# Kernel tuning notes

Hardware: AMD Instinct MI355X
Metric: run time of the kernel (lower is better)

Reference implementation:

```python
import jax, jax.numpy as jnp
import numpy as np

D_MODEL = 1024
D_FF = 4 * D_MODEL
N = D_MODEL * D_FF          # 4,194,304 == 2**22, so pad_n == N (no padding)
PAD_N = N
FFT_LEN = PAD_N // 2 + 1    # 2,097,153 rfft bins
KEEP = int(FFT_LEN * 0.25)  # 524,288 kept coefficients ('medium')
B, S = 4, 2048


def _decompress(cr, ci, idx, shape, scale):
    # scatter top-k complex coeffs into full rfft spectrum, inverse rfft,
    # reshape to weight matrix and rescale (riemann_decompress)
    coeffs = jax.lax.complex(cr, ci)                      # complex64 [KEEP]
    full = jnp.zeros((FFT_LEN,), jnp.complex64).at[idx].set(coeffs)
    w = jnp.fft.irfft(full, n=PAD_N)                      # [PAD_N] real
    return w.reshape(shape) * scale                       # scale is [1], broadcasts


def setup_inputs() -> dict:
    key = jax.random.key(0)
    ks = jax.random.split(key, 9)
    return {
        "x": jax.random.normal(ks[0], (B, S, D_MODEL), jnp.float32),
        "c_fc_coeffs_real": jax.random.normal(ks[1], (KEEP,), jnp.float32),
        "c_fc_coeffs_imag": jax.random.normal(ks[2], (KEEP,), jnp.float32),
        "c_fc_indices": jnp.arange(KEEP, dtype=jnp.int32),
        "c_fc_scale": jax.random.uniform(ks[3], (1,), jnp.float32, 0.5, 1.5),
        "c_fc_bias": jax.random.normal(ks[4], (D_FF,), jnp.float32),
        "c_proj_coeffs_real": jax.random.normal(ks[5], (KEEP,), jnp.float32),
        "c_proj_coeffs_imag": jax.random.normal(ks[6], (KEEP,), jnp.float32),
        "c_proj_indices": jnp.arange(KEEP, dtype=jnp.int32),
        "c_proj_scale": jax.random.uniform(ks[7], (1,), jnp.float32, 0.5, 1.5),
        "c_proj_bias": jax.random.normal(ks[8], (D_MODEL,), jnp.float32),
    }


def reference(x, c_fc_coeffs_real, c_fc_coeffs_imag, c_fc_indices, c_fc_scale,
              c_fc_bias, c_proj_coeffs_real, c_proj_coeffs_imag, c_proj_indices,
              c_proj_scale, c_proj_bias):
    # c_fc.weight stored [d_model, d_ff]; F.linear(x, W.T) == x @ W
    w_fc = _decompress(c_fc_coeffs_real, c_fc_coeffs_imag, c_fc_indices,
                       (D_MODEL, D_FF), c_fc_scale)
    h = jnp.einsum('bsd,df->bsf', x, w_fc) + c_fc_bias
    h = jax.nn.gelu(h, approximate=False)  # nn.GELU() exact erf form
    w_proj = _decompress(c_proj_coeffs_real, c_proj_coeffs_imag, c_proj_indices,
                         (D_FF, D_MODEL), c_proj_scale)
    return jnp.einsum('bsf,fd->bsd', h, w_proj) + c_proj_bias
```

## Files before the change

### kernel.cpp

```cpp
#include <hip/hip_runtime.h>
#include <hip/hip_bf16.h>
#include <hip/hip_fp8.h>
#include <math.h>

#define M_HALF 2097152
#define W_SCALE 256.0f

typedef __bf16 bf16_t;
typedef unsigned char u8;
typedef __attribute__((ext_vector_type(4))) float f32x4;
typedef __attribute__((ext_vector_type(2))) long long2v;

#define GLOBAL_AS __attribute__((address_space(1)))
#define LDS_AS    __attribute__((address_space(3)))

__device__ __forceinline__ u8 to_fp8(float v) {
    __hip_fp8_e4m3 t(v);
    return *reinterpret_cast<u8*>(&t);
}

__device__ __forceinline__ int perm8(int g) {
    return (((g >> 3) * 4 + (g & 3)) << 1) + ((g >> 2) & 1);
}
__device__ __forceinline__ int permk(int k) {
    return (k & ~127) | (perm8((k >> 3) & 15) * 8 + (k & 7));
}

__device__ __forceinline__ float2 cadd(float2 a, float2 b){ return make_float2(a.x+b.x, a.y+b.y); }
__device__ __forceinline__ float2 csub(float2 a, float2 b){ return make_float2(a.x-b.x, a.y-b.y); }
__device__ __forceinline__ float2 cmul(float2 a, float2 b){ return make_float2(a.x*b.x-a.y*b.y, a.x*b.y+a.y*b.x); }
__device__ __forceinline__ float2 cmuli(float2 a){ return make_float2(-a.y, a.x); }

__device__ __forceinline__ void radix8_inv(const float2 v[8], float2 X[8]) {
    const float cc = 0.70710678118654752f;
    float2 a0 = cadd(v[0], v[4]), a1 = cadd(v[1], v[5]), a2 = cadd(v[2], v[6]), a3 = cadd(v[3], v[7]);
    float2 b0 = csub(v[0], v[4]), b1 = csub(v[1], v[5]), b2 = csub(v[2], v[6]), b3 = csub(v[3], v[7]);
    b1 = cmul(b1, make_float2(cc, cc));
    b2 = cmuli(b2);
    b3 = cmul(b3, make_float2(-cc, cc));
    float2 c0 = cadd(a0, a2), c1 = cadd(a1, a3), d0 = csub(a0, a2), d1 = cmuli(csub(a1, a3));
    float2 e0 = cadd(b0, b2), e1 = cadd(b1, b3), f0 = csub(b0, b2), f1 = cmuli(csub(b1, b3));
    X[0] = cadd(c0, c1); X[4] = csub(c0, c1); X[2] = cadd(d0, d1); X[6] = csub(d0, d1);
    X[1] = cadd(e0, e1); X[5] = csub(e0, e1); X[3] = cadd(f0, f1); X[7] = csub(f0, f1);
}


__global__ __launch_bounds__(256) void zero2_kernel(float2* p, int n) {
    int i = blockIdx.x*256 + threadIdx.x;
    if (i < n) p[i] = make_float2(0.f, 0.f);
}

__global__ __launch_bounds__(256) void scatter2_kernel(const float* __restrict__ crA,
                                                       const float* __restrict__ ciA,
                                                       const int* __restrict__ idxA,
                                                       const float* __restrict__ crB,
                                                       const float* __restrict__ ciB,
                                                       const int* __restrict__ idxB,
                                                       float2* __restrict__ specA,
                                                       float2* __restrict__ specB, int keep) {
    int i = blockIdx.x*256 + threadIdx.x;
    if (i < keep) {
        int k = idxA[i];
        long pos = (k < M_HALF) ? ((long)(k & 511)*4096 + (k >> 9)) : (long)M_HALF;
        specA[pos] = make_float2(crA[i], ciA[i]);
    } else if (i < 2*keep) {
        int t = i - keep;
        int k = idxB[t];
        long pos = (k < M_HALF) ? ((long)(k & 511)*4096 + (k >> 9)) : (long)M_HALF;
        specB[pos] = make_float2(crB[t], ciB[t]);
    }
}


__global__ __launch_bounds__(512) void ifft_p4096_dual(const float2* __restrict__ specTA,
                                                       const float2* __restrict__ specTB,
                                                       float2* __restrict__ dstA,
                                                       float2* __restrict__ dstB,
                                                       const float* __restrict__ scaleA,
                                                       const float* __restrict__ scaleB) {
    __shared__ float2 L[8*656];
    int bb = blockIdx.x;
    const float2* spec; float2* dst; const float* scale;
    if (bb < 512) { spec = specTA; dst = dstA; scale = scaleA; }
    else          { bb -= 512; spec = specTB; dst = dstB; scale = scaleB; }
    const int j = bb;
    const int x = threadIdx.x;
    const float s = scale[0] * (1.0f/(float)M_HALF);
    float2 v[8];
    {
        float ang0 = (float)(3.14159265358979323846 * (double)(j + 512*x) / 2097152.0);
        float sn, cs; sincosf(ang0, &sn, &cs);
        const float2 step = make_float2(0.98078528040323044913f,
                                        0.19509032201612826785f);
        float2 tw = make_float2(cs, sn);
        const long arow = (long)j * 4096;
        const long brow = (long)(512 - j) * 4096;
#pragma unroll
        for (int u = 0; u < 8; ++u) {
            int t = x + 512*u;
            float2 a = spec[arow + t];
            float2 b;
            if (j == 0) b = (t == 0) ? spec[(long)M_HALF] : spec[4096 - t];
            else        b = spec[brow + 4095 - t];
            if (j == 0 && t == 0) { a.y = 0.0f; b.y = 0.0f; }
            float Er = 0.5f*(a.x + b.x), Ei = 0.5f*(a.y - b.y);
            float Tr = 0.5f*(a.x - b.x), Ti = 0.5f*(a.y + b.y);
            float Or = Tr*tw.x - Ti*tw.y, Oi = Tr*tw.y + Ti*tw.x;
            v[u] = make_float2((Er - Oi)*s, (Ei + Or)*s);
            tw = cmul(tw, step);
        }
    }
    float2 E[8];
    radix8_inv(v, E);
    {
        float cb, sb; sincosf((float)x * 0.0015339807878856412f, &sb, &cb);
        float2 wb = make_float2(cb, sb), w = make_float2(1.f, 0.f);
#pragma unroll
        for (int a = 0; a < 8; ++a) { L[a*656 + x] = cmul(E[a], w); w = cmul(w, wb); }
    }
    __syncthreads();
    const int g = x >> 6, xin = x & 63;
    float2* Lg = L + g*656;
    float2 v2[8];
#pragma unroll
    for (int u2 = 0; u2 < 8; ++u2) v2[u2] = Lg[xin + 64*u2];
    float2 E2[8];
    radix8_inv(v2, E2);
    __syncthreads();
    {
        float cb, sb; sincosf((float)xin * 0.012271846303085130f, &sb, &cb);
        float2 wb = make_float2(cb, sb), w = make_float2(1.f, 0.f);
#pragma unroll
        for (int s8 = 0; s8 < 8; ++s8) { Lg[s8*65 + xin] = cmul(E2[s8], w); w = cmul(w, wb); }
    }
    __syncthreads();
    const int p = xin >> 3, xa = xin & 7;
    float2 g2[8];
#pragma unroll
    for (int xb = 0; xb < 8; ++xb) g2[xb] = Lg[p*65 + xa + 8*xb];
    float2 H2[8];
    radix8_inv(g2, H2);
    __syncthreads();
    {
        float cb, sb; sincosf((float)xa * 0.098174770424681039f, &sb, &cb);
        float2 wb = make_float2(cb, sb), w = make_float2(1.f, 0.f);
#pragma unroll
        for (int o8 = 0; o8 < 8; ++o8) { Lg[p*81 + o8*9 + xa] = cmul(H2[o8], w); w = cmul(w, wb); }
    }
    __syncthreads();
    const int pp = xin & 7, sp = xin >> 3;
    float2 r2[8];
#pragma unroll
    for (int xa2 = 0; xa2 < 8; ++xa2) r2[xa2] = Lg[pp*81 + sp*9 + xa2];
    float2 D[8];
    radix8_inv(r2, D);
    __syncthreads();
#pragma unroll
    for (int ob = 0; ob < 8; ++ob) {
        int sg = g + 8*xin + 512*ob;
        L[sg ^ ((sg >> 4) & 7)] = D[ob];
    }
    __syncthreads();
    const long obase = (long)j * 4096;
#pragma unroll
    for (int e = 0; e < 8; ++e) {
        int idx = x + 512*e;
        dst[obase + idx] = L[idx ^ ((idx >> 4) & 7)];
    }
}


__global__ __launch_bounds__(512) void ifft_p512f8_dual(const float2* __restrict__ srcA,
                                                        u8* __restrict__ dstwA,
                                                        const float2* __restrict__ srcB,
                                                        u8* __restrict__ dstwB) {
    __shared__ float2 ex[8 * 642];
    int bb = blockIdx.x;
    const float2* src; u8* dstw; bool isA;
    if (bb < 512) { src = srcA; dstw = dstwA; isA = true; }
    else          { bb -= 512; src = srcB; dstw = dstwB; isA = false; }
    const int tid = threadIdx.x;
    const int jl = tid & 7, x = tid >> 3;
    const int jg = bb * 8 + jl;
    float2* W = ex + jl * 642;
    float2 v[8];
    {
        float a0 = (float)(6.283185307179586 * (double)jg * (double)x / 2097152.0);
        float sn0, cs0; sincosf(a0, &sn0, &cs0);
        float as = (float)(6.283185307179586 * (double)jg / 32768.0);
        float sns, css; sincosf(as, &sns, &css);
        float2 tw = make_float2(cs0, sn0), stepw = make_float2(css, sns);
#pragma unroll
        for (int u = 0; u < 8; ++u) {
            v[u] = cmul(src[jg + (long)(x + 64*u) * 4096], tw);
            tw = cmul(tw, stepw);
        }
    }
    float2 E[8];
    radix8_inv(v, E);
    {
        float cb, sb; sincosf((float)x * 0.012271846303085130f, &sb, &cb);
        float2 wb = make_float2(cb, sb), w = make_float2(1.f, 0.f);
#pragma unroll
        for (int s8 = 0; s8 < 8; ++s8) {
            W[s8*65 + x] = cmul(E[s8], w);
            w = cmul(w, wb);
        }
    }
    __syncthreads();
    const int p = x >> 3, xa = x & 7;
    float2 g[8];
#pragma unroll
    for (int xb = 0; xb < 8; ++xb) g[xb] = W[p*65 + xa + 8*xb];
    float2 H[8];
    radix8_inv(g, H);
    __syncthreads();
    {
        float cb, sb; sincosf((float)xa * 0.098174770424681039f, &sb, &cb);
        float2 wb = make_float2(cb, sb), w = make_float2(1.f, 0.f);
#pragma unroll
        for (int o8 = 0; o8 < 8; ++o8) {
            W[p*81 + o8*9 + xa] = cmul(H[o8], w);
            w = cmul(w, wb);
        }
    }
    __syncthreads();
    const int pp = x & 7, sp = x >> 3;
    float2 r[8];
#pragma unroll
    for (int xa2 = 0; xa2 < 8; ++xa2) r[xa2] = W[pp*81 + sp*9 + xa2];
    float2 Y[8];
    radix8_inv(r, Y);
#pragma unroll
    for (int ob = 0; ob < 8; ++ob) {
        int sidx = x + 64*ob;
        long n2;
        if (isA) {
            int rr = 2*sidx + (jg >> 11);
            n2 = (long)permk(rr) * 2048 + (jg & 2047);
        } else {
            int rr = 8*sidx + (jg >> 9);
            n2 = (long)permk(rr) * 512 + (jg & 511);
        }
        unsigned short pk = (unsigned short)to_fp8(Y[ob].x * W_SCALE) |
                            ((unsigned short)to_fp8(Y[ob].y * W_SCALE) << 8);
        ((unsigned short*)dstw)[n2] = pk;
    }
}


__global__ __launch_bounds__(256) void transpose_f8_dual(const u8* __restrict__ wA,
                                                         u8* __restrict__ wTA,
                                                         const u8* __restrict__ wB,
                                                         u8* __restrict__ wTB) {
    __shared__ u8 tile[32][36];
    int b = blockIdx.x;
    const u8* w; u8* wT; int R, C, bx, by;
    if (b < 4096) { w = wA; wT = wTA; R = 1024; C = 4096; bx = b & 127; by = b >> 7; }
    else { b -= 4096; w = wB; wT = wTB; R = 4096; C = 1024; bx = b & 31; by = b >> 5; }
    int tx = threadIdx.x & 31, ty = threadIdx.x >> 5;
    long c0 = (long)bx * 32, r0 = (long)by * 32;
#pragma unroll
    for (int i = 0; i < 4; ++i)
        tile[ty + i*8][tx] = w[(r0 + ty + i*8) * C + c0 + tx];
    __syncthreads();
#pragma unroll
    for (int i = 0; i < 4; ++i) {
        int c = ty + i*8;
        wT[(c0 + c) * R + r0 + tx] = tile[tx][c];
    }
}


__global__ __launch_bounds__(256) void cvt_fp8_kernel(const float* __restrict__ in,
                                                      u8* __restrict__ out, int n8) {
    int i = blockIdx.x*256 + threadIdx.x;
    if (i < n8) {
        float4 v0 = ((const float4*)in)[i*2];
        float4 v1 = ((const float4*)in)[i*2+1];
        unsigned long pk =  (unsigned long)to_fp8(v0.x)
                         | ((unsigned long)to_fp8(v0.y) << 8)
                         | ((unsigned long)to_fp8(v0.z) << 16)
                         | ((unsigned long)to_fp8(v0.w) << 24)
                         | ((unsigned long)to_fp8(v1.x) << 32)
                         | ((unsigned long)to_fp8(v1.y) << 40)
                         | ((unsigned long)to_fp8(v1.z) << 48)
                         | ((unsigned long)to_fp8(v1.w) << 56);
        ((unsigned long*)out)[(i >> 4) * 16 + perm8(i & 15)] = pk;
    }
}


template<int NITER>
__device__ __forceinline__ void stage_b(const u8* g, int ldB, int row0, int col0B,
                                        u8* lds, int tid) {
    int w = tid >> 6, l = tid & 63;
    int r8 = l >> 3;
    int cg = ((l & 7) ^ r8) << 4;
#pragma unroll
    for (int i = 0; i < NITER; ++i) {
        int chunk = (i << 3) + w;
        const u8* ga = g + (long)(row0 + chunk*8 + r8) * ldB + col0B + cg;
        u8* la = lds + (chunk << 10);
        __builtin_amdgcn_global_load_lds((const GLOBAL_AS unsigned int*)ga,
                                         (LDS_AS unsigned int*)la, 16, 0, 0);
    }
}


template<int EPI>
__global__ __launch_bounds__(512, 6) void gemm_f8(const u8* __restrict__ A,
                                                  const u8* __restrict__ Bt,
                                                  const float* __restrict__ bias,
                                                  void* __restrict__ Cout,
                                                  int M, int N, int K,
                                                  int CR, int CC, int GXC) {
    __shared__ __align__(16) u8 lA[128*128];
    __shared__ __align__(16) u8 lB[128*128];
    const int tid = threadIdx.x;
    const int l = tid & 63, w = tid >> 6;
    const int wr = w >> 2, wc = w & 3;
    int flat = blockIdx.y * gridDim.x + blockIdx.x;
    int r = flat & 7, q = flat >> 3;
    int ty = (r / GXC) * CR + q / CC;
    int tx = (r % GXC) * CC + q % CC;
    const int row0 = ty * 128, col0 = tx * 128;
    const int lr = l & 15, lq = l >> 4;
    const int xr = (lr & 7) << 4;
    f32x4 acc[4][2] = {};
    for (int k0 = 0; k0 < K; k0 += 128) {
        stage_b<2>(A,  K, row0, k0, lA, tid);
        stage_b<2>(Bt, K, col0, k0, lB, tid);
        __syncthreads();
#pragma unroll
        for (int kk2 = 0; kk2 < 2; ++kk2) {
            long2v af[4], bfr[2];
            const int kb = (kk2*64 + lq*16) ^ xr;
#pragma unroll
            for (int mi = 0; mi < 4; ++mi)
                af[mi] = *(const long2v*)(lA + (wr*64 + mi*16 + lr)*128 + kb);
#pragma unroll
            for (int ni = 0; ni < 2; ++ni)
                bfr[ni] = *(const long2v*)(lB + (wc*32 + ni*16 + lr)*128 + kb);
#pragma unroll
            for (int mi = 0; mi < 4; ++mi)
#pragma unroll
                for (int ni = 0; ni < 2; ++ni) {
                    acc[mi][ni] = __builtin_amdgcn_mfma_f32_16x16x32_fp8_fp8(
                        af[mi][0], bfr[ni][0], acc[mi][ni], 0, 0, 0);
                    acc[mi][ni] = __builtin_amdgcn_mfma_f32_16x16x32_fp8_fp8(
                        af[mi][1], bfr[ni][1], acc[mi][ni], 0, 0, 0);
                }
        }
        __syncthreads();
    }
    const float inv_s = 1.0f / W_SCALE;
#pragma unroll
    for (int mi = 0; mi < 4; ++mi) {
#pragma unroll
        for (int ni = 0; ni < 2; ++ni) {
            int c = col0 + wc*32 + ni*16 + lr;
            float bv = bias[c];
#pragma unroll
            for (int q2 = 0; q2 < 4; ++q2) {
                int rr = row0 + wr*64 + mi*16 + lq*4 + q2;
                float v = acc[mi][ni][q2] * inv_s + bv;
                if constexpr (EPI == 0) {
                    float y = -1.5957691216057308f * (v + 0.044715f * v * v * v);
                    v = v / (1.0f + __expf(y));
                    ((u8*)Cout)[(long)rr * N + permk(c)] = to_fp8(v);
                } else {
                    ((float*)Cout)[(long)rr * N + c] = v;
                }
            }
        }
    }
}


extern "C" void kernel_launch(void* const* d_in, const int* in_sizes, int n_in,
                              void* d_out, int out_size, void* d_ws, size_t ws_size,
                              hipStream_t stream) {
    const float* x        = (const float*)d_in[0];
    const float* fc_cr    = (const float*)d_in[1];
    const float* fc_ci    = (const float*)d_in[2];
    const int*   fc_idx   = (const int*)  d_in[3];
    const float* fc_scale = (const float*)d_in[4];
    const float* fc_bias  = (const float*)d_in[5];
    const float* pj_cr    = (const float*)d_in[6];
    const float* pj_ci    = (const float*)d_in[7];
    const int*   pj_idx   = (const int*)  d_in[8];
    const float* pj_scale = (const float*)d_in[9];
    const float* pj_bias  = (const float*)d_in[10];
    const int keep = in_sizes[1];

    char* ws = (char*)d_ws;
    u8* w_fcT = (u8*)(ws + 0);
    u8* w_pjT = (u8*)(ws + 4194304);
    u8* x_f8  = (u8*)(ws + 8388608);
    u8* h_f8  = (u8*)(ws + 16777216);
    const long SP = (long)M_HALF + 64;
    float2* specA = (float2*)(ws + 8388608);
    float2* specB = specA + SP;
    float2* fftA_A = (float2*)(ws + 50331648);
    float2* fftA_B = (float2*)(ws + 67108864);
    u8* w_natA = (u8*)(ws + 8388608);
    u8* w_natB = (u8*)(ws + 12582912);

    zero2_kernel<<<(int)((2*SP + 255)/256), 256, 0, stream>>>(specA, (int)(2*SP));
    scatter2_kernel<<<(2*keep + 255)/256, 256, 0, stream>>>(
        fc_cr, fc_ci, fc_idx, pj_cr, pj_ci, pj_idx, specA, specB, keep);
    ifft_p4096_dual<<<1024, 512, 0, stream>>>(specA, specB, fftA_A, fftA_B,
                                              fc_scale, pj_scale);
    ifft_p512f8_dual<<<1024, 512, 0, stream>>>(fftA_A, w_natA, fftA_B, w_natB);
    transpose_f8_dual<<<8192, 256, 0, stream>>>(w_natA, w_fcT, w_natB, w_pjT);

    cvt_fp8_kernel<<<8388608/8/256, 256, 0, stream>>>(x, x_f8, 8388608/8);

    gemm_f8<0><<<dim3(4096/128, 8192/128), 512, 0, stream>>>(
        x_f8, w_fcT, fc_bias, h_f8, 8192, 4096, 1024, 16, 16, 2);

    gemm_f8<1><<<dim3(1024/128, 8192/128), 512, 0, stream>>>(
        h_f8, w_pjT, pj_bias, d_out, 8192, 1024, 4096, 8, 8, 1);

    (void)n_in; (void)out_size; (void)ws_size;
}
```

Baseline: 186.6 us.

## Use MI355 scaled 16x16x128 FP8 MFMA with a matching K permutation

Replaces the pairs of 16x16x32 fp8 MFMAs with the gfx950 scaled 16x16x128 f8f6f4 MFMA, which uses unit scales (0x7F exponent). Each lane now gathers two 16-byte LDS chunks into an 8-int operand. The perm8 K-permutation used when writing the fp8 activations changes to match the new operand lane layout. The aim is to issue fewer, wider MFMA instructions per K-tile, at the cost of depending on the exact K-ordering semantics of the new instruction and holding more register pressure for operands.

Result: faster. 170.3 us (-8.7%).

```diff
diff --git a/kernel.cpp b/kernel.cpp
--- a/kernel.cpp
+++ b/kernel.cpp
@@ -9,7 +9,8 @@
 typedef __bf16 bf16_t;
 typedef unsigned char u8;
 typedef __attribute__((ext_vector_type(4))) float f32x4;
-typedef __attribute__((ext_vector_type(2))) long long2v;
+typedef __attribute__((ext_vector_type(4))) int   i32x4;
+typedef __attribute__((ext_vector_type(8))) int   i32x8;
 
 #define GLOBAL_AS __attribute__((address_space(1)))
 #define LDS_AS    __attribute__((address_space(3)))
@@ -20,7 +21,7 @@
 }
 
 __device__ __forceinline__ int perm8(int g) {
-    return (((g >> 3) * 4 + (g & 3)) << 1) + ((g >> 2) & 1);
+    return ((g & 2) << 2) | ((g & 12) >> 1) | (g & 1);
 }
 __device__ __forceinline__ int permk(int k) {
     return (k & ~127) | (perm8((k >> 3) & 15) * 8 + (k & 7));
@@ -327,30 +328,40 @@
     const int row0 = ty * 128, col0 = tx * 128;
     const int lr = l & 15, lq = l >> 4;
     const int xr = (lr & 7) << 4;
+    const int kb0 = (lq*16) ^ xr;
+    const int kb1 = (64 + lq*16) ^ xr;
     f32x4 acc[4][2] = {};
     for (int k0 = 0; k0 < K; k0 += 128) {
         stage_b<2>(A,  K, row0, k0, lA, tid);
         stage_b<2>(Bt, K, col0, k0, lB, tid);
         __syncthreads();
-#pragma unroll
-        for (int kk2 = 0; kk2 < 2; ++kk2) {
-            long2v af[4], bfr[2];
-            const int kb = (kk2*64 + lq*16) ^ xr;
-#pragma unroll
-            for (int mi = 0; mi < 4; ++mi)
-                af[mi] = *(const long2v*)(lA + (wr*64 + mi*16 + lr)*128 + kb);
-#pragma unroll
-            for (int ni = 0; ni < 2; ++ni)
-                bfr[ni] = *(const long2v*)(lB + (wc*32 + ni*16 + lr)*128 + kb);
-#pragma unroll
-            for (int mi = 0; mi < 4; ++mi)
-#pragma unroll
-                for (int ni = 0; ni < 2; ++ni) {
-                    acc[mi][ni] = __builtin_amdgcn_mfma_f32_16x16x32_fp8_fp8(
-                        af[mi][0], bfr[ni][0], acc[mi][ni], 0, 0, 0);
-                    acc[mi][ni] = __builtin_amdgcn_mfma_f32_16x16x32_fp8_fp8(
-                        af[mi][1], bfr[ni][1], acc[mi][ni], 0, 0, 0);
-                }
+        i32x8 bfr[2];
+#pragma unroll
+        for (int ni = 0; ni < 2; ++ni) {
+            const u8* rp = lB + (wc*32 + ni*16 + lr)*128;
+            i32x4 lo = *(const i32x4*)(rp + kb0);
+            i32x4 hi = *(const i32x4*)(rp + kb1);
+            bfr[ni] = __builtin_shufflevector(lo, hi, 0, 1, 2, 3, 4, 5, 6, 7);
+        }
+#pragma unroll
+        for (int mh = 0; mh < 2; ++mh) {
+            i32x8 af[2];
+#pragma unroll
+            for (int m2 = 0; m2 < 2; ++m2) {
+                const u8* rp = lA + (wr*64 + (mh*2 + m2)*16 + lr)*128;
+                i32x4 lo = *(const i32x4*)(rp + kb0);
+                i32x4 hi = *(const i32x4*)(rp + kb1);
+                af[m2] = __builtin_shufflevector(lo, hi, 0, 1, 2, 3, 4, 5, 6, 7);
+            }
+#pragma unroll
+            for (int m2 = 0; m2 < 2; ++m2)
+#pragma unroll
+                for (int ni = 0; ni < 2; ++ni)
+                    acc[mh*2 + m2][ni] = __builtin_amdgcn_mfma_scale_f32_16x16x128_f8f6f4(
+                        af[m2], bfr[ni], acc[mh*2 + m2][ni],
+                        0, 0,
+                        0, 0x7F7F7F7F,
+                        0, 0x7F7F7F7F);
         }
         __syncthreads();
     }
```
